# Kernel optimization log

Hardware: AMD Instinct MI355X
Metric: run time of the kernel (lower is better)

## Reference

```python
import jax, jax.numpy as jnp
import numpy as np

N = 50000          # nodes
DEG = 8            # per-node in/out degree
E = N * DEG        # fwd edges (rev = reversed fwd)
H = 128            # hidden_dim
T = 4              # towers
F = H // T         # per-tower F_in (divide_input=True)
FO = H // T        # per-tower F_out
L = 2              # num_layers
IN_DIM = 128
OUT_DIM = 32
AVG_LOG = float(np.log(DEG + 1.0))  # avg of log(deg+1) from deg histogram (all deg==8)
BN_EPS = 1e-5
STD_EPS = 1e-5


def setup_inputs() -> dict:
    key = jax.random.key(0)
    ks = jax.random.split(key, 10)
    x = jax.random.normal(ks[0], (N, IN_DIM), jnp.float32)
    # every node appears exactly DEG times as dst and as src -> deg histogram delta at 8
    dst = jnp.repeat(jnp.arange(N, dtype=jnp.int32), DEG)
    src = jax.random.permutation(ks[1], dst)
    edge_fwd = jnp.stack([src, dst])  # [2, E]

    def rn(k, shape):
        return jax.random.normal(k, shape, jnp.float32) * 0.05

    return dict(
        x=x,
        W_in=rn(ks[2], (IN_DIM, H)), b_in=jnp.zeros((H,), jnp.float32),
        # [layer, relation(fwd/rev), tower, ...]
        pre_W=rn(ks[3], (L, 2, T, 2 * F, F)), pre_b=jnp.zeros((L, 2, T, F), jnp.float32),
        post_W=rn(ks[4], (L, 2, T, 13 * F, FO)), post_b=jnp.zeros((L, 2, T, FO), jnp.float32),
        lin_W=rn(ks[5], (L, 2, H, H)), lin_b=jnp.zeros((L, 2, H), jnp.float32),
        bn_gamma=jnp.ones((L, H), jnp.float32), bn_beta=jnp.zeros((L, H), jnp.float32),
        mlp_W1=rn(ks[6], (H, H)), mlp_b1=jnp.zeros((H,), jnp.float32),
        mlp_W2=rn(ks[7], (H, OUT_DIM)), mlp_b2=jnp.zeros((OUT_DIM,), jnp.float32),
        edge_fwd=edge_fwd,
    )


def _pna(x, src, dst, pre_W, pre_b, post_W, post_b, lin_W, lin_b):
    """One PNAConv (divide_input=True, pre/post_layers=1, no edge attr)."""
    xt = x.reshape(N, T, F)                                   # [N,T,F]
    # message: cat([x_i (dst), x_j (src)]) -> per-tower pre-MLP
    h = jnp.concatenate([xt[dst], xt[src]], axis=-1)          # [E,T,2F]
    m = jnp.einsum('etf,tfg->etg', h, pre_W) + pre_b          # [E,T,F]
    # multi-aggregator scatter reduce over destination nodes
    deg = jax.ops.segment_sum(jnp.ones((m.shape[0],), x.dtype), dst, N)
    degc = jnp.maximum(deg, 1.0)
    inv = (1.0 / degc)[:, None, None]
    mean = jax.ops.segment_sum(m, dst, N) * inv
    mean2 = jax.ops.segment_sum(m * m, dst, N) * inv
    std = jnp.sqrt(jax.nn.relu(mean2 - mean * mean) + STD_EPS)
    mn = jax.ops.segment_min(m, dst, N)
    mx = jax.ops.segment_max(m, dst, N)
    agg = jnp.concatenate([mean, mn, mx, std], axis=-1)       # [N,T,4F]
    # degree scalers: amplification, attenuation, identity
    ld = jnp.log(degc + 1.0)[:, None, None]
    agg = jnp.concatenate([agg * (ld / AVG_LOG), agg * (AVG_LOG / ld), agg], axis=-1)  # [N,T,12F]
    out = jnp.concatenate([xt, agg], axis=-1)                 # [N,T,13F]
    out = jnp.einsum('ntf,tfg->ntg', out, post_W) + post_b    # [N,T,FO]
    out = out.reshape(N, T * FO)
    return out @ lin_W + lin_b                                # [N,H]


def _bn(x, g, b):
    mu = x.mean(0)
    var = x.var(0)  # biased, as torch BatchNorm normalization
    return g * (x - mu) * jax.lax.rsqrt(var + BN_EPS) + b


def reference(x, W_in, b_in, pre_W, pre_b, post_W, post_b, lin_W, lin_b,
              bn_gamma, bn_beta, mlp_W1, mlp_b1, mlp_W2, mlp_b2, edge_fwd):
    src, dst = edge_fwd[0], edge_fwd[1]
    h = jax.nn.relu(x @ W_in + b_in)
    for l in range(L):
        # HeteroConv sum of fwd relation and rev relation (reversed edges)
        y = (_pna(h, src, dst, pre_W[l, 0], pre_b[l, 0], post_W[l, 0], post_b[l, 0], lin_W[l, 0], lin_b[l, 0])
             + _pna(h, dst, src, pre_W[l, 1], pre_b[l, 1], post_W[l, 1], post_b[l, 1], lin_W[l, 1], lin_b[l, 1]))
        h = jax.nn.relu(_bn(y, bn_gamma[l], bn_beta[l]))
        # dropout omitted (deterministic reference / eval mode)
    return jax.nn.relu(h @ mlp_W1 + mlp_b1) @ mlp_W2 + mlp_b2
```

## Files before the change

### kernel.cpp

```cpp
#include <hip/hip_runtime.h>
#include <hip/hip_fp16.h>
#include <cstddef>
#include <cstdint>

#define NN 50000
#define DEG 8
#define EE (NN*DEG)
#define RT_CNT 3125
#define AG_CNT 1563
#define KSTEPS 36
#define W8L 18432
#define MPAD 132

typedef __attribute__((ext_vector_type(8))) short short8;
typedef __attribute__((ext_vector_type(4))) float f32x4;

union Pack8 { __half h[8]; __half2 h2[4]; uint4 u; short8 s8; };

__global__ void k_build_nbr(const int* __restrict__ ef, int* __restrict__ cnt,
                            int* __restrict__ rev_nbr) {
    int e = blockIdx.x * blockDim.x + threadIdx.x;
    if (e >= EE) return;
    int s = ef[e], d = ef[EE + e];
    int q = atomicAdd(&cnt[s], 1);
    rev_nbr[s * DEG + q] = d;
}

__global__ __launch_bounds__(256) void k_wprep(
    const float* __restrict__ post_W, const float* __restrict__ pre_W,
    const float* __restrict__ pre_b, const float* __restrict__ post_b,
    const float* __restrict__ lin_W, const float* __restrict__ lin_b,
    __half* __restrict__ Wcp, float* __restrict__ Qw, float* __restrict__ bc) {
    __shared__ float Pf[160 * 33];
    __shared__ float Wl[32 * 128];
    __shared__ float Wt[32 * 32];
    __shared__ float Ps[32 * 32];
    __shared__ float Q[32 * 32];
    __shared__ float T3s[32];
    int tid = threadIdx.x;
    int m4 = blockIdx.x;
    int l = m4 >> 3, r = (m4 >> 2) & 1, tw = m4 & 3;
    const float* PW = post_W + (size_t)m4 * 416 * 32;
    for (int i = tid; i < 160 * 32; i += 256) {
        int row = i >> 5, g = i & 31;
        float v;
        if (row < 32) v = PW[row * 32 + g];
        else {
            int rr = row - 32;
            v = PW[(32 + rr) * 32 + g] + PW[(160 + rr) * 32 + g] + PW[(288 + rr) * 32 + g];
        }
        Pf[row * 33 + g] = v;
    }
    for (int i = tid; i < 1024; i += 256) Wt[i] = pre_W[(size_t)m4 * 2048 + i];
    for (int i = tid; i < 4096; i += 256)
        Wl[i] = lin_W[(size_t)(l * 2 + r) * 16384 + tw * 32 * 128 + i];
    __syncthreads();
    for (int i = tid; i < 1024; i += 256) {
        int g = i >> 5, j = i & 31;
        Ps[i] = Pf[(32 + g) * 33 + j] + Pf[(64 + g) * 33 + j] + Pf[(96 + g) * 33 + j];
    }
    __syncthreads();
    for (int i = tid; i < 1024; i += 256) {
        int f = i >> 5, j = i & 31;
        float acc = Pf[f * 33 + j];
#pragma unroll
        for (int g = 0; g < 32; g++) acc += Wt[f * 32 + g] * Ps[g * 32 + j];
        Q[i] = acc;
    }
    if (tid < 32) {
        int j = tid;
        float v = post_b[m4 * 32 + j];
#pragma unroll
        for (int g = 0; g < 32; g++) v += pre_b[m4 * 32 + g] * Ps[g * 32 + j];
        T3s[j] = v;
    }
    __syncthreads();
    for (int u = tid; u < 2048; u += 256) {
        int lane = u & 63, t = (u >> 6) & 7, s = u >> 9;
        int quad = lane >> 4, nl = lane & 15;
        int n = t * 16 + nl;
        Pack8 pk;
#pragma unroll
        for (int e = 0; e < 8; e++) {
            int f = quad * 8 + e;
            const float* Pr = &Pf[((s + 1) * 32 + f) * 33];
            float acc = 0.f;
#pragma unroll
            for (int j = 0; j < 32; j++) acc += Pr[j] * Wl[j * 128 + n];
            pk.h[e] = __float2half(acc);
        }
        int ks = 4 + r * 16 + tw * 4 + s;
        *(uint4*)&Wcp[((size_t)l * W8L + (t * KSTEPS + ks) * 64 + lane) * 8] = pk.u;
    }
    for (int i = tid; i < 4096; i += 256) {
        int f = i >> 7, n = i & 127;
        float acc = 0.f;
#pragma unroll
        for (int j = 0; j < 32; j++) acc += Q[f * 32 + j] * Wl[j * 128 + n];
        atomicAdd(&Qw[(size_t)l * 16384 + (tw * 32 + f) * 128 + n], acc);
    }
    if (tid < 128) {
        float v = 0.f;
#pragma unroll
        for (int j = 0; j < 32; j++) v += T3s[j] * Wl[j * 128 + tid];
        atomicAdd(&bc[l * 128 + tid], v);
        if ((m4 & 7) == 0)
            atomicAdd(&bc[l * 128 + tid],
                      lin_b[(2 * l) * 128 + tid] + lin_b[(2 * l + 1) * 128 + tid]);
    }
}

__global__ void k_pack_all(const float* __restrict__ Qw, __half* __restrict__ Wcp,
                           const float* __restrict__ W_in, __half* __restrict__ Winp,
                           const float* __restrict__ mlp_W1, __half* __restrict__ W1p,
                           const float* __restrict__ mlp_W2, __half* __restrict__ W2p,
                           const float* __restrict__ pre_W, __half* __restrict__ WbBD) {
    int gid = blockIdx.x * blockDim.x + threadIdx.x;
    if (gid < 4096) {
        int lane = gid & 63, t = (gid >> 6) & 7, ks = (gid >> 9) & 3, l = gid >> 11;
        int quad = lane >> 4;
        int n = t * 16 + (lane & 15);
        Pack8 pk;
#pragma unroll
        for (int e = 0; e < 8; e++)
            pk.h[e] = __float2half(Qw[(size_t)l * 16384 + (ks * 32 + quad * 8 + e) * 128 + n]);
        *(uint4*)&Wcp[((size_t)l * W8L + (t * KSTEPS + ks) * 64 + lane) * 8] = pk.u;
        return;
    }
    if (gid < 8704) {
        const float* W; __half* dst; int id, Kq;
        if (gid < 6144)      { W = W_in;   dst = Winp; id = gid - 4096; Kq = 4; }
        else if (gid < 8192) { W = mlp_W1; dst = W1p;  id = gid - 6144; Kq = 4; }
        else                 { W = mlp_W2; dst = W2p;  id = gid - 8192; Kq = 4; }
        int N = (gid < 8192) ? 128 : 32;
        int lane = id & 63;
        int ks = (id >> 6) % Kq;
        int t = (id >> 6) / Kq;
        int quad = lane >> 4, nl = lane & 15;
        int n = t * 16 + nl;
        Pack8 pk;
#pragma unroll
        for (int e = 0; e < 8; e++)
            pk.h[e] = __float2half(W[(size_t)(ks * 32 + quad * 8 + e) * N + n]);
        *(uint4*)&dst[(size_t)id * 8] = pk.u;
        return;
    }
    {
        int id = gid - 8704;
        int lane = id & 63, ks = (id >> 6) & 3, t8 = (id >> 8) & 7;
        int rel = (id >> 11) & 1, l = id >> 12;
        int quad = lane >> 4, nl = lane & 15;
        int n = t8 * 16 + nl;
        int tn = n >> 5;
        Pack8 pk;
#pragma unroll
        for (int e = 0; e < 8; e++) {
            int k = ks * 32 + quad * 8 + e;
            float v = 0.f;
            if ((k >> 5) == tn)
                v = pre_W[(size_t)((((l * 2 + rel) * 4 + tn) * 64) + 32 + (k & 31)) * 32 + (n & 31)];
            pk.h[e] = __float2half(v);
        }
        *(uint4*)&WbBD[((size_t)(l * 2 + rel) * 2048 + (t8 * 4 + ks) * 64 + lane) * 8] = pk.u;
    }
}

__global__ __launch_bounds__(256) void k_in_fused(
    const float* __restrict__ X, const __half* __restrict__ Wp,
    const float* __restrict__ b, const __half* __restrict__ WbBDp,
    __half* __restrict__ H, __half* __restrict__ Bplanes) {
    __shared__ __half Sh[4][16 * MPAD];
    int tid = threadIdx.x, wv = tid >> 6, lane = tid & 63;
    int rt = blockIdx.x * 4 + wv;
    if (rt >= RT_CNT) rt = RT_CNT - 1;
    int mm = lane & 15, quad = lane >> 4;
    short8 a[4];
#pragma unroll
    for (int ks = 0; ks < 4; ks++) {
        const float4* p = (const float4*)&X[(size_t)(rt * 16 + mm) * 128 + ks * 32 + quad * 8];
        float4 v0 = p[0], v1 = p[1];
        Pack8 pk;
        pk.h[0] = __float2half(v0.x); pk.h[1] = __float2half(v0.y);
        pk.h[2] = __float2half(v0.z); pk.h[3] = __float2half(v0.w);
        pk.h[4] = __float2half(v1.x); pk.h[5] = __float2half(v1.y);
        pk.h[6] = __float2half(v1.z); pk.h[7] = __float2half(v1.w);
        a[ks] = pk.s8;
    }
    const short8* Bb = (const short8*)Wp + lane;
    f32x4 acc[8];
#pragma unroll
    for (int t = 0; t < 8; t++) acc[t] = (f32x4){0.f, 0.f, 0.f, 0.f};
#pragma unroll
    for (int ks = 0; ks < 4; ks++)
#pragma unroll
        for (int t = 0; t < 8; t++)
            acc[t] = __builtin_amdgcn_mfma_f32_16x16x32_f16(
                a[ks], Bb[(t * 4 + ks) * 64], acc[t], 0, 0, 0);
    __half* T = Sh[wv];
#pragma unroll
    for (int t = 0; t < 8; t++) {
        int n = t * 16 + mm;
        float bias = b[n];
#pragma unroll
        for (int r = 0; r < 4; r++)
            T[(quad * 4 + r) * MPAD + n] = __float2half(fmaxf(acc[t][r] + bias, 0.f));
    }
#pragma unroll
    for (int it = 0; it < 4; it++) {
        int idx = it * 64 + lane;
        int row = idx >> 4, col = (idx & 15) * 8;
        *(uint4*)&H[(size_t)(rt * 16 + row) * 128 + col] = *(uint4*)&T[row * MPAD + col];
    }
    short8 a2[4];
#pragma unroll
    for (int ks = 0; ks < 4; ks++)
        a2[ks] = *(const short8*)&T[mm * MPAD + ks * 32 + quad * 8];
#pragma unroll
    for (int rel = 0; rel < 2; rel++) {
        const short8* Bd = (const short8*)WbBDp + (size_t)rel * 2048 + lane;
        f32x4 ac[8];
#pragma unroll
        for (int t = 0; t < 8; t++) ac[t] = (f32x4){0.f, 0.f, 0.f, 0.f};
#pragma unroll
        for (int ks = 0; ks < 4; ks++)
#pragma unroll
            for (int t = 0; t < 8; t++)
                ac[t] = __builtin_amdgcn_mfma_f32_16x16x32_f16(
                    a2[ks], Bd[(t * 4 + ks) * 64], ac[t], 0, 0, 0);
#pragma unroll
        for (int t = 0; t < 8; t++) {
            int n = t * 16 + mm;
#pragma unroll
            for (int r = 0; r < 4; r++)
                T[(quad * 4 + r) * MPAD + n] = __float2half(ac[t][r]);
        }
        __half* Bp = Bplanes + (size_t)rel * NN * 128;
#pragma unroll
        for (int it = 0; it < 4; it++) {
            int idx = it * 64 + lane;
            int row = idx >> 4, col = (idx & 15) * 8;
            *(uint4*)&Bp[(size_t)(rt * 16 + row) * 128 + col] = *(uint4*)&T[row * MPAD + col];
        }
    }
}

template<int V>
__global__ __launch_bounds__(256) void k_preB_mfma(
    const __half* __restrict__ Hin, const float* __restrict__ Yf,
    const float* __restrict__ bns, const float* __restrict__ bns2,
    const float* __restrict__ gamma, const float* __restrict__ beta,
    __half* __restrict__ Hout, const __half* __restrict__ WbBDp,
    __half* __restrict__ Bplanes) {
    __shared__ __half Sh[4][16 * MPAD];
    __shared__ float sc[128], sh[128];
    int tid = threadIdx.x, wv = tid >> 6, lane = tid & 63;
    int rt = blockIdx.x * 4 + wv;
    if (rt >= RT_CNT) rt = RT_CNT - 1;
    if (V == 2) {
        if (tid < 128) {
            float mu = bns[tid] * (1.f / NN);
            float var = bns2[tid] * (1.f / NN) - mu * mu;
            float s = gamma[tid] * rsqrtf(var + 1e-5f);
            sc[tid] = s;
            sh[tid] = beta[tid] - mu * s;
        }
        __syncthreads();
    }
    int mm = lane & 15, quad = lane >> 4;
    short8 a[4];
#pragma unroll
    for (int ks = 0; ks < 4; ks++) {
        int c0 = ks * 32 + quad * 8;
        size_t base = (size_t)(rt * 16 + mm) * 128 + c0;
        if (V == 1) {
            Pack8 pk; pk.u = *(const uint4*)&Hin[base];
            a[ks] = pk.s8;
        } else {
            const float4* p = (const float4*)&Yf[base];
            float4 v0 = p[0], v1 = p[1];
            float4 s0 = *(const float4*)&sc[c0], s1 = *(const float4*)&sc[c0 + 4];
            float4 f0 = *(const float4*)&sh[c0], f1 = *(const float4*)&sh[c0 + 4];
            Pack8 pk;
            pk.h[0] = __float2half(fmaxf(s0.x * v0.x + f0.x, 0.f));
            pk.h[1] = __float2half(fmaxf(s0.y * v0.y + f0.y, 0.f));
            pk.h[2] = __float2half(fmaxf(s0.z * v0.z + f0.z, 0.f));
            pk.h[3] = __float2half(fmaxf(s0.w * v0.w + f0.w, 0.f));
            pk.h[4] = __float2half(fmaxf(s1.x * v1.x + f1.x, 0.f));
            pk.h[5] = __float2half(fmaxf(s1.y * v1.y + f1.y, 0.f));
            pk.h[6] = __float2half(fmaxf(s1.z * v1.z + f1.z, 0.f));
            pk.h[7] = __float2half(fmaxf(s1.w * v1.w + f1.w, 0.f));
            *(uint4*)&Hout[base] = pk.u;
            a[ks] = pk.s8;
        }
    }
    __half* T = Sh[wv];
#pragma unroll
    for (int rel = 0; rel < 2; rel++) {
        const short8* Bb = (const short8*)WbBDp + (size_t)rel * 2048 + lane;
        f32x4 acc[8];
#pragma unroll
        for (int t = 0; t < 8; t++) acc[t] = (f32x4){0.f, 0.f, 0.f, 0.f};
#pragma unroll
        for (int ks = 0; ks < 4; ks++)
#pragma unroll
            for (int t = 0; t < 8; t++)
                acc[t] = __builtin_amdgcn_mfma_f32_16x16x32_f16(
                    a[ks], Bb[(t * 4 + ks) * 64], acc[t], 0, 0, 0);
#pragma unroll
        for (int t = 0; t < 8; t++) {
            int n = t * 16 + mm;
#pragma unroll
            for (int r = 0; r < 4; r++)
                T[(quad * 4 + r) * MPAD + n] = __float2half(acc[t][r]);
        }
        __half* Bp = Bplanes + (size_t)rel * NN * 128;
#pragma unroll
        for (int it = 0; it < 4; it++) {
            int idx = it * 64 + lane;
            int row = idx >> 4, col = (idx & 15) * 8;
            *(uint4*)&Bp[(size_t)(rt * 16 + row) * 128 + col] = *(uint4*)&T[row * MPAD + col];
        }
    }
}

__global__ __launch_bounds__(512) void k_agg_gemm(
    const __half* __restrict__ hbuf, const __half* __restrict__ Bplanes,
    const int* __restrict__ fwd_nbr, const int* __restrict__ rev_nbr,
    const __half* __restrict__ Wcp, const float* __restrict__ bc,
    float* __restrict__ Y, float* __restrict__ bnsum, float* __restrict__ bnsum2) {
    __shared__ __half Spack[32 * 128 * 8];
    int tid = threadIdx.x;
    int blk = blockIdx.x;
    int lane = tid & 63, wv = tid >> 6;
    int G = tid >> 4;
    int f16 = tid & 15;
    int tw = f16 >> 2, quad = f16 & 3;
    int fo = f16 * 8;
    int pos = quad * 32 + (G ^ quad ^ ((tw & 1) << 2));
    int mB = lane & 15, qB = lane >> 4;
    int t = wv;
    int nodeg = blk * 32 + G;
    if (nodeg >= NN) nodeg = NN - 1;

    Pack8 axt[2][4];
#pragma unroll
    for (int mt = 0; mt < 2; mt++) {
        int nd = blk * 32 + mt * 16 + mB;
        if (nd >= NN) nd = NN - 1;
#pragma unroll
        for (int ks = 0; ks < 4; ks++)
            axt[mt][ks].u = *(const uint4*)&hbuf[(size_t)nd * 128 + ks * 32 + qB * 8];
    }
    {
        const int4* nf = (const int4*)&fwd_nbr[nodeg * 8];
        const int4* nr = (const int4*)&rev_nbr[nodeg * 8];
        int4 a0 = nf[0], a1 = nf[1], b0v = nr[0], b1v = nr[1];
        int idx0[8] = {a0.x, a0.y, a0.z, a0.w, a1.x, a1.y, a1.z, a1.w};
        int idx1[8] = {b0v.x, b0v.y, b0v.z, b0v.w, b1v.x, b1v.y, b1v.z, b1v.w};
        Pack8 r0[8], r1[8];
        const __half* Bp1 = Bplanes + (size_t)NN * 128;
#pragma unroll
        for (int k = 0; k < 8; k++)
            r0[k].u = *(const uint4*)&Bplanes[(size_t)idx0[k] * 128 + fo];
#pragma unroll
        for (int k = 0; k < 8; k++)
            r1[k].u = *(const uint4*)&Bp1[(size_t)idx1[k] * 128 + fo];
#pragma unroll
        for (int rel = 0; rel < 2; rel++) {
            Pack8* rr = rel ? r1 : r0;
            float sS[8], qS[8], mnS[8], mxS[8];
#pragma unroll
            for (int j = 0; j < 8; j++) {
                sS[j] = 0.f; qS[j] = 0.f; mnS[j] = 1e30f; mxS[j] = -1e30f;
            }
#pragma unroll
            for (int k = 0; k < 8; k++) {
#pragma unroll
                for (int j2 = 0; j2 < 4; j2++) {
                    __half2 h = rr[k].h2[j2];
                    float a = __half2float(__low2half(h));
                    float b = __half2float(__high2half(h));
                    int j0 = 2 * j2, j1 = j0 + 1;
                    sS[j0] += a; qS[j0] += a * a;
                    mnS[j0] = fminf(mnS[j0], a); mxS[j0] = fmaxf(mxS[j0], a);
                    sS[j1] += b; qS[j1] += b * b;
                    mnS[j1] = fminf(mnS[j1], b); mxS[j1] = fmaxf(mxS[j1], b);
                }
            }
            Pack8 mean, stdv, mnp, mxp;
#pragma unroll
            for (int j = 0; j < 8; j++) {
                float Bm = sS[j] * 0.125f;
                mean.h[j] = __float2half(Bm);
                stdv.h[j] = __float2half(
                    sqrtf(fmaxf(qS[j] * 0.125f - Bm * Bm, 0.f) + 1e-5f));
                mnp.h[j] = __float2half(mnS[j]);
                mxp.h[j] = __float2half(mxS[j]);
            }
            int ksb = rel * 16 + tw * 4;
            *(uint4*)&Spack[((size_t)(ksb + 0) * 128 + pos) * 8] = mean.u;
            *(uint4*)&Spack[((size_t)(ksb + 1) * 128 + pos) * 8] = mnp.u;
            *(uint4*)&Spack[((size_t)(ksb + 2) * 128 + pos) * 8] = mxp.u;
            *(uint4*)&Spack[((size_t)(ksb + 3) * 128 + pos) * 8] = stdv.u;
        }
    }
    __syncthreads();
    const short8* Bb = (const short8*)Wcp + lane;
    f32x4 acc0 = (f32x4){0.f, 0.f, 0.f, 0.f};
    f32x4 acc1 = (f32x4){0.f, 0.f, 0.f, 0.f};
    short8 p[6];
#pragma unroll
    for (int dd = 0; dd < 6; dd++) p[dd] = Bb[((size_t)t * KSTEPS + dd) * 64];
    __builtin_amdgcn_s_setprio(1);
#pragma unroll
    for (int ks = 0; ks < KSTEPS; ks++) {
        short8 a0f, a1f;
        if (ks < 4) {
            a0f = axt[0][ks].s8;
            a1f = axt[1][ks].s8;
        } else {
            int ss = ks - 4;
            int twk = (ss >> 2) & 3;
            int posr = qB * 32 + (mB ^ qB ^ ((twk & 1) << 2));
            const __half* row = &Spack[((size_t)ss * 128 + posr) * 8];
            a0f = *(const short8*)row;
            a1f = *(const short8*)(row + 16 * 8);
        }
        acc0 = __builtin_amdgcn_mfma_f32_16x16x32_f16(a0f, p[ks % 6], acc0, 0, 0, 0);
        acc1 = __builtin_amdgcn_mfma_f32_16x16x32_f16(a1f, p[ks % 6], acc1, 0, 0, 0);
        if (ks + 6 < KSTEPS) p[ks % 6] = Bb[((size_t)t * KSTEPS + ks + 6) * 64];
    }
    __builtin_amdgcn_s_setprio(0);
#pragma unroll
    for (int mt = 0; mt < 2; mt++) {
        f32x4 acc = mt ? acc1 : acc0;
        int n = t * 16 + mB;
        float bias = bc[n];
        float ls = 0.f, ls2 = 0.f;
#pragma unroll
        for (int r = 0; r < 4; r++) {
            int node = blk * 32 + mt * 16 + qB * 4 + r;
            if (node < NN) {
                float v = acc[r] + bias;
                Y[(size_t)node * 128 + n] = v;
                ls += v; ls2 += v * v;
            }
        }
        ls += __shfl_xor(ls, 16); ls += __shfl_xor(ls, 32);
        ls2 += __shfl_xor(ls2, 16); ls2 += __shfl_xor(ls2, 32);
        if (qB == 0) {
            atomicAdd(&bnsum[n], ls);
            atomicAdd(&bnsum2[n], ls2);
        }
    }
}

__global__ __launch_bounds__(256) void k_mlp_mfma(
    const float* __restrict__ Yb, const float* __restrict__ bns,
    const float* __restrict__ bns2, const float* __restrict__ gamma,
    const float* __restrict__ beta, const __half* __restrict__ W1p,
    const float* __restrict__ b1, const __half* __restrict__ W2p,
    const float* __restrict__ b2, float* __restrict__ out) {
    __shared__ __half Sh[4][16 * MPAD];
    __shared__ float sc[128], sh[128];
    int tid = threadIdx.x, wv = tid >> 6, lane = tid & 63;
    int rt = blockIdx.x * 4 + wv;
    if (rt >= RT_CNT) rt = RT_CNT - 1;
    if (tid < 128) {
        float mu = bns[tid] * (1.f / NN);
        float var = bns2[tid] * (1.f / NN) - mu * mu;
        float s = gamma[tid] * rsqrtf(var + 1e-5f);
        sc[tid] = s;
        sh[tid] = beta[tid] - mu * s;
    }
    __syncthreads();
    int mm = lane & 15, quad = lane >> 4;
    short8 a[4];
#pragma unroll
    for (int ks = 0; ks < 4; ks++) {
        int c0 = ks * 32 + quad * 8;
        const float4* p = (const float4*)&Yb[(size_t)(rt * 16 + mm) * 128 + c0];
        float4 v0 = p[0], v1 = p[1];
        float4 s0 = *(const float4*)&sc[c0], s1 = *(const float4*)&sc[c0 + 4];
        float4 f0 = *(const float4*)&sh[c0], f1 = *(const float4*)&sh[c0 + 4];
        Pack8 pk;
        pk.h[0] = __float2half(fmaxf(s0.x * v0.x + f0.x, 0.f));
        pk.h[1] = __float2half(fmaxf(s0.y * v0.y + f0.y, 0.f));
        pk.h[2] = __float2half(fmaxf(s0.z * v0.z + f0.z, 0.f));
        pk.h[3] = __float2half(fmaxf(s0.w * v0.w + f0.w, 0.f));
        pk.h[4] = __float2half(fmaxf(s1.x * v1.x + f1.x, 0.f));
        pk.h[5] = __float2half(fmaxf(s1.y * v1.y + f1.y, 0.f));
        pk.h[6] = __float2half(fmaxf(s1.z * v1.z + f1.z, 0.f));
        pk.h[7] = __float2half(fmaxf(s1.w * v1.w + f1.w, 0.f));
        a[ks] = pk.s8;
    }
    const short8* B1 = (const short8*)W1p + lane;
    f32x4 acc[8];
#pragma unroll
    for (int t = 0; t < 8; t++) acc[t] = (f32x4){0.f, 0.f, 0.f, 0.f};
#pragma unroll
    for (int ks = 0; ks < 4; ks++)
#pragma unroll
        for (int t = 0; t < 8; t++)
            acc[t] = __builtin_amdgcn_mfma_f32_16x16x32_f16(
                a[ks], B1[(t * 4 + ks) * 64], acc[t], 0, 0, 0);
    __half* T = Sh[wv];
#pragma unroll
    for (int t = 0; t < 8; t++) {
        int n = t * 16 + mm;
        float bias = b1[n];
#pragma unroll
        for (int r = 0; r < 4; r++)
            T[(quad * 4 + r) * MPAD + n] = __float2half(fmaxf(acc[t][r] + bias, 0.f));
    }
    short8 a2[4];
#pragma unroll
    for (int ks = 0; ks < 4; ks++)
        a2[ks] = *(const short8*)&T[mm * MPAD + ks * 32 + quad * 8];
    const short8* B2 = (const short8*)W2p + lane;
    f32x4 acc2[2];
#pragma unroll
    for (int t = 0; t < 2; t++) acc2[t] = (f32x4){0.f, 0.f, 0.f, 0.f};
#pragma unroll
    for (int ks = 0; ks < 4; ks++)
#pragma unroll
        for (int t = 0; t < 2; t++)
            acc2[t] = __builtin_amdgcn_mfma_f32_16x16x32_f16(
                a2[ks], B2[(t * 4 + ks) * 64], acc2[t], 0, 0, 0);
#pragma unroll
    for (int t = 0; t < 2; t++) {
        int n = t * 16 + mm;
        float bias = b2[n];
#pragma unroll
        for (int r = 0; r < 4; r++)
            out[(size_t)(rt * 16 + quad * 4 + r) * 32 + n] = acc2[t][r] + bias;
    }
}

extern "C" void kernel_launch(void* const* d_in, const int* in_sizes, int n_in,
                              void* d_out, int out_size, void* d_ws, size_t ws_size,
                              hipStream_t stream) {
    const float* x      = (const float*)d_in[0];
    const float* W_in   = (const float*)d_in[1];
    const float* b_in   = (const float*)d_in[2];
    const float* pre_W  = (const float*)d_in[3];
    const float* pre_b  = (const float*)d_in[4];
    const float* post_W = (const float*)d_in[5];
    const float* post_b = (const float*)d_in[6];
    const float* lin_W  = (const float*)d_in[7];
    const float* lin_b  = (const float*)d_in[8];
    const float* bn_g   = (const float*)d_in[9];
    const float* bn_b   = (const float*)d_in[10];
    const float* mlp_W1 = (const float*)d_in[11];
    const float* mlp_b1 = (const float*)d_in[12];
    const float* mlp_W2 = (const float*)d_in[13];
    const float* mlp_b2 = (const float*)d_in[14];
    const int*   edge   = (const int*)d_in[15];
    float* out = (float*)d_out;

    char* w = (char*)d_ws;
    const size_t plane = (size_t)NN * 128 * sizeof(float);
    __half* hbuf = (__half*)w; w += plane / 2;
    float* ybuf = (float*)w; w += plane;
    __half* Bpl = (__half*)w; w += plane;
    int* rev_nbr = (int*)w; w += (size_t)NN * DEG * sizeof(int);
    char* zbase = w;
    int* cnt     = (int*)w; w += (size_t)NN * sizeof(int);
    float* Qw    = (float*)w; w += (size_t)2 * 128 * 128 * sizeof(float);
    float* bc    = (float*)w; w += 2 * 128 * sizeof(float);
    float* bns   = (float*)w; w += 4 * 128 * sizeof(float);
    size_t zsize = (size_t)(w - zbase);
    __half* Wcp  = (__half*)w; w += (size_t)2 * KSTEPS * 32 * 128 * sizeof(__half);
    __half* Winp = (__half*)w; w += (size_t)128 * 128 * sizeof(__half);
    __half* W1p  = (__half*)w; w += (size_t)128 * 128 * sizeof(__half);
    __half* W2p  = (__half*)w; w += (size_t)128 * 32 * sizeof(__half);
    __half* WbBD = (__half*)w; w += (size_t)4 * 128 * 128 * sizeof(__half);

    const int gWave = (RT_CNT + 3) / 4;
    const int* fwd_nbr = edge;

    (void)hipMemsetAsync(zbase, 0, zsize, stream);
    k_build_nbr<<<(EE + 255) / 256, 256, 0, stream>>>(edge, cnt, rev_nbr);
    k_wprep<<<16, 256, 0, stream>>>(post_W, pre_W, pre_b, post_b, lin_W, lin_b,
                                    Wcp, Qw, bc);
    k_pack_all<<<66, 256, 0, stream>>>(Qw, Wcp, W_in, Winp, mlp_W1, W1p,
                                       mlp_W2, W2p, pre_W, WbBD);

    k_in_fused<<<gWave, 256, 0, stream>>>(x, Winp, b_in, WbBD, hbuf, Bpl);

    k_agg_gemm<<<AG_CNT, 512, 0, stream>>>(
        hbuf, Bpl, fwd_nbr, rev_nbr, Wcp, bc, ybuf, bns, bns + 128);
    k_preB_mfma<2><<<gWave, 256, 0, stream>>>(
        nullptr, ybuf, bns, bns + 128, bn_g, bn_b, hbuf,
        WbBD + (size_t)2 * 128 * 128, Bpl);
    k_agg_gemm<<<AG_CNT, 512, 0, stream>>>(
        hbuf, Bpl, fwd_nbr, rev_nbr, Wcp + (size_t)KSTEPS * 32 * 128,
        bc + 128, ybuf, bns + 256, bns + 384);

    k_mlp_mfma<<<gWave, 256, 0, stream>>>(ybuf, bns + 256, bns + 384,
                                          bn_g + 128, bn_b + 128,
                                          W1p, mlp_b1, W2p, mlp_b2, out);
}
```

Before: 418.2 us.

## Merge graph build, weight prep and packing into fewer kernel launches

Folds the neighbor-list build, the weight preprocessing and the independent weight packing into one k_prep launch. The Qw-dependent packing moves into extra blocks appended to k_in_fused, which removes two kernel launches and their serialization gaps. The build now also constructs an explicit fwd_nbr list through a second atomic counter instead of reading the edge array directly. That adds extra atomics, a larger zeroed region and a new 1.6MB buffer, and it may change neighbor ordering.

```diff
diff --git a/kernel.cpp b/kernel.cpp
--- a/kernel.cpp
+++ b/kernel.cpp
@@ -11,26 +11,25 @@
 #define KSTEPS 36
 #define W8L 18432
 #define MPAD 132
+#define BUILD_BLKS 1563
+#define PREP_BLKS (16 + BUILD_BLKS + 50)
 
 typedef __attribute__((ext_vector_type(8))) short short8;
 typedef __attribute__((ext_vector_type(4))) float f32x4;
 
 union Pack8 { __half h[8]; __half2 h2[4]; uint4 u; short8 s8; };
 
-__global__ void k_build_nbr(const int* __restrict__ ef, int* __restrict__ cnt,
-                            int* __restrict__ rev_nbr) {
-    int e = blockIdx.x * blockDim.x + threadIdx.x;
-    if (e >= EE) return;
-    int s = ef[e], d = ef[EE + e];
-    int q = atomicAdd(&cnt[s], 1);
-    rev_nbr[s * DEG + q] = d;
-}
-
-__global__ __launch_bounds__(256) void k_wprep(
+__global__ __launch_bounds__(256) void k_prep(
     const float* __restrict__ post_W, const float* __restrict__ pre_W,
     const float* __restrict__ pre_b, const float* __restrict__ post_b,
     const float* __restrict__ lin_W, const float* __restrict__ lin_b,
-    __half* __restrict__ Wcp, float* __restrict__ Qw, float* __restrict__ bc) {
+    __half* __restrict__ Wcp, float* __restrict__ Qw, float* __restrict__ bc,
+    const int* __restrict__ ef, int* __restrict__ cnt,
+    int* __restrict__ fwd_nbr, int* __restrict__ rev_nbr,
+    const float* __restrict__ W_in, __half* __restrict__ Winp,
+    const float* __restrict__ mlp_W1, __half* __restrict__ W1p,
+    const float* __restrict__ mlp_W2, __half* __restrict__ W2p,
+    __half* __restrict__ WbBD) {
     __shared__ float Pf[160 * 33];
     __shared__ float Wl[32 * 128];
     __shared__ float Wt[32 * 32];
@@ -38,7 +37,56 @@
     __shared__ float Q[32 * 32];
     __shared__ float T3s[32];
     int tid = threadIdx.x;
-    int m4 = blockIdx.x;
+    int b = blockIdx.x;
+    if (b >= 16 && b < 16 + BUILD_BLKS) {
+        int e = (b - 16) * 256 + tid;
+        if (e < EE) {
+            int s = ef[e], d = ef[EE + e];
+            int p = atomicAdd(&cnt[d], 1);
+            fwd_nbr[d * DEG + p] = s;
+            int q = atomicAdd(&cnt[NN + s], 1);
+            rev_nbr[s * DEG + q] = d;
+        }
+        return;
+    }
+    if (b >= 16 + BUILD_BLKS) {
+        int pid = (b - 16 - BUILD_BLKS) * 256 + tid;
+        if (pid < 4608) {
+            const float* W; __half* dst; int id; int N;
+            if (pid < 2048)      { W = W_in;   dst = Winp; id = pid;        N = 128; }
+            else if (pid < 4096) { W = mlp_W1; dst = W1p;  id = pid - 2048; N = 128; }
+            else                 { W = mlp_W2; dst = W2p;  id = pid - 4096; N = 32;  }
+            int lane = id & 63;
+            int ks = (id >> 6) & 3;
+            int t = (id >> 6) >> 2;
+            int quad = lane >> 4, nl = lane & 15;
+            int n = t * 16 + nl;
+            Pack8 pk;
+#pragma unroll
+            for (int e = 0; e < 8; e++)
+                pk.h[e] = __float2half(W[(size_t)(ks * 32 + quad * 8 + e) * N + n]);
+            *(uint4*)&dst[(size_t)id * 8] = pk.u;
+        } else if (pid < 12800) {
+            int id = pid - 4608;
+            int lane = id & 63, ks = (id >> 6) & 3, t8 = (id >> 8) & 7;
+            int rel = (id >> 11) & 1, l = id >> 12;
+            int quad = lane >> 4, nl = lane & 15;
+            int n = t8 * 16 + nl;
+            int tn = n >> 5;
+            Pack8 pk;
+#pragma unroll
+            for (int e = 0; e < 8; e++) {
+                int k = ks * 32 + quad * 8 + e;
+                float v = 0.f;
+                if ((k >> 5) == tn)
+                    v = pre_W[(size_t)((((l * 2 + rel) * 4 + tn) * 64) + 32 + (k & 31)) * 32 + (n & 31)];
+                pk.h[e] = __float2half(v);
+            }
+            *(uint4*)&WbBD[((size_t)(l * 2 + rel) * 2048 + (t8 * 4 + ks) * 64 + lane) * 8] = pk.u;
+        }
+        return;
+    }
+    int m4 = b;
     int l = m4 >> 3, r = (m4 >> 2) & 1, tw = m4 & 3;
     const float* PW = post_W + (size_t)m4 * 416 * 32;
     for (int i = tid; i < 160 * 32; i += 256) {
@@ -110,67 +158,27 @@
     }
 }
 
-__global__ void k_pack_all(const float* __restrict__ Qw, __half* __restrict__ Wcp,
-                           const float* __restrict__ W_in, __half* __restrict__ Winp,
-                           const float* __restrict__ mlp_W1, __half* __restrict__ W1p,
-                           const float* __restrict__ mlp_W2, __half* __restrict__ W2p,
-                           const float* __restrict__ pre_W, __half* __restrict__ WbBD) {
-    int gid = blockIdx.x * blockDim.x + threadIdx.x;
-    if (gid < 4096) {
-        int lane = gid & 63, t = (gid >> 6) & 7, ks = (gid >> 9) & 3, l = gid >> 11;
-        int quad = lane >> 4;
-        int n = t * 16 + (lane & 15);
-        Pack8 pk;
-#pragma unroll
-        for (int e = 0; e < 8; e++)
-            pk.h[e] = __float2half(Qw[(size_t)l * 16384 + (ks * 32 + quad * 8 + e) * 128 + n]);
-        *(uint4*)&Wcp[((size_t)l * W8L + (t * KSTEPS + ks) * 64 + lane) * 8] = pk.u;
-        return;
-    }
-    if (gid < 8704) {
-        const float* W; __half* dst; int id, Kq;
-        if (gid < 6144)      { W = W_in;   dst = Winp; id = gid - 4096; Kq = 4; }
-        else if (gid < 8192) { W = mlp_W1; dst = W1p;  id = gid - 6144; Kq = 4; }
-        else                 { W = mlp_W2; dst = W2p;  id = gid - 8192; Kq = 4; }
-        int N = (gid < 8192) ? 128 : 32;
-        int lane = id & 63;
-        int ks = (id >> 6) % Kq;
-        int t = (id >> 6) / Kq;
-        int quad = lane >> 4, nl = lane & 15;
-        int n = t * 16 + nl;
-        Pack8 pk;
-#pragma unroll
-        for (int e = 0; e < 8; e++)
-            pk.h[e] = __float2half(W[(size_t)(ks * 32 + quad * 8 + e) * N + n]);
-        *(uint4*)&dst[(size_t)id * 8] = pk.u;
-        return;
-    }
-    {
-        int id = gid - 8704;
-        int lane = id & 63, ks = (id >> 6) & 3, t8 = (id >> 8) & 7;
-        int rel = (id >> 11) & 1, l = id >> 12;
-        int quad = lane >> 4, nl = lane & 15;
-        int n = t8 * 16 + nl;
-        int tn = n >> 5;
-        Pack8 pk;
-#pragma unroll
-        for (int e = 0; e < 8; e++) {
-            int k = ks * 32 + quad * 8 + e;
-            float v = 0.f;
-            if ((k >> 5) == tn)
-                v = pre_W[(size_t)((((l * 2 + rel) * 4 + tn) * 64) + 32 + (k & 31)) * 32 + (n & 31)];
-            pk.h[e] = __float2half(v);
-        }
-        *(uint4*)&WbBD[((size_t)(l * 2 + rel) * 2048 + (t8 * 4 + ks) * 64 + lane) * 8] = pk.u;
-    }
-}
-
 __global__ __launch_bounds__(256) void k_in_fused(
     const float* __restrict__ X, const __half* __restrict__ Wp,
     const float* __restrict__ b, const __half* __restrict__ WbBDp,
-    __half* __restrict__ H, __half* __restrict__ Bplanes) {
+    __half* __restrict__ H, __half* __restrict__ Bplanes,
+    const float* __restrict__ Qw, __half* __restrict__ Wcp, int gWave) {
     __shared__ __half Sh[4][16 * MPAD];
     int tid = threadIdx.x, wv = tid >> 6, lane = tid & 63;
+    if (blockIdx.x >= gWave) {
+        int gid = (blockIdx.x - gWave) * 256 + tid;
+        if (gid < 4096) {
+            int pl = gid & 63, t = (gid >> 6) & 7, ks = (gid >> 9) & 3, l = gid >> 11;
+            int quad = pl >> 4;
+            int n = t * 16 + (pl & 15);
+            Pack8 pk;
+#pragma unroll
+            for (int e = 0; e < 8; e++)
+                pk.h[e] = __float2half(Qw[(size_t)l * 16384 + (ks * 32 + quad * 8 + e) * 128 + n]);
+            *(uint4*)&Wcp[((size_t)l * W8L + (t * KSTEPS + ks) * 64 + pl) * 8] = pk.u;
+        }
+        return;
+    }
     int rt = blockIdx.x * 4 + wv;
     if (rt >= RT_CNT) rt = RT_CNT - 1;
     int mm = lane & 15, quad = lane >> 4;
@@ -563,9 +571,10 @@
     __half* hbuf = (__half*)w; w += plane / 2;
     float* ybuf = (float*)w; w += plane;
     __half* Bpl = (__half*)w; w += plane;
+    int* fwd_nbr = (int*)w; w += (size_t)NN * DEG * sizeof(int);
     int* rev_nbr = (int*)w; w += (size_t)NN * DEG * sizeof(int);
     char* zbase = w;
-    int* cnt     = (int*)w; w += (size_t)NN * sizeof(int);
+    int* cnt     = (int*)w; w += (size_t)2 * NN * sizeof(int);
     float* Qw    = (float*)w; w += (size_t)2 * 128 * 128 * sizeof(float);
     float* bc    = (float*)w; w += 2 * 128 * sizeof(float);
     float* bns   = (float*)w; w += 4 * 128 * sizeof(float);
@@ -577,16 +586,15 @@
     __half* WbBD = (__half*)w; w += (size_t)4 * 128 * 128 * sizeof(__half);
 
     const int gWave = (RT_CNT + 3) / 4;
-    const int* fwd_nbr = edge;
 
     (void)hipMemsetAsync(zbase, 0, zsize, stream);
-    k_build_nbr<<<(EE + 255) / 256, 256, 0, stream>>>(edge, cnt, rev_nbr);
-    k_wprep<<<16, 256, 0, stream>>>(post_W, pre_W, pre_b, post_b, lin_W, lin_b,
-                                    Wcp, Qw, bc);
-    k_pack_all<<<66, 256, 0, stream>>>(Qw, Wcp, W_in, Winp, mlp_W1, W1p,
-                                       mlp_W2, W2p, pre_W, WbBD);
-
-    k_in_fused<<<gWave, 256, 0, stream>>>(x, Winp, b_in, WbBD, hbuf, Bpl);
+    k_prep<<<PREP_BLKS, 256, 0, stream>>>(
+        post_W, pre_W, pre_b, post_b, lin_W, lin_b, Wcp, Qw, bc,
+        edge, cnt, fwd_nbr, rev_nbr,
+        W_in, Winp, mlp_W1, W1p, mlp_W2, W2p, WbBD);
+
+    k_in_fused<<<gWave + 16, 256, 0, stream>>>(x, Winp, b_in, WbBD, hbuf, Bpl,
+                                               Qw, Wcp, gWave);
 
     k_agg_gemm<<<AG_CNT, 512, 0, stream>>>(
         hbuf, Bpl, fwd_nbr, rev_nbr, Wcp, bc, ybuf, bns, bns + 128);
```

Measured after the change: 436.5 us. +4.4%, slower.
